# Optimization experiments

Hardware: AMD Instinct MI355X
Metric: run time of the kernel (lower is better)

## Reference

```python
import jax, jax.numpy as jnp
import numpy as np

B, T, EMB, HS = 512, 256, 364, 64

def setup_inputs() -> dict:
    key = jax.random.key(0)
    ks = jax.random.split(key, 7)
    s = EMB ** -0.5  # keep weight scale sane
    return {
        "x": jax.random.normal(ks[0], (B, T, EMB), jnp.float32),
        "Wk": jax.random.normal(ks[1], (EMB, HS), jnp.float32) * s,
        "bk": jax.random.normal(ks[2], (HS,), jnp.float32) * 0.01,
        "Wq": jax.random.normal(ks[3], (EMB, HS), jnp.float32) * s,
        "bq": jax.random.normal(ks[4], (HS,), jnp.float32) * 0.01,
        "Wv": jax.random.normal(ks[5], (EMB, HS), jnp.float32) * s,
        "bv": jax.random.normal(ks[6], (HS,), jnp.float32) * 0.01,
    }

def reference(x, Wk, bk, Wq, bq, Wv, bv):
    # Faithful to the original: wei = k @ q^T (note swapped q/k vs textbook),
    # scaled by head_size**-0.5, causal mask, softmax, (dropout = identity in eval), then @ v.
    k = x @ Wk + bk          # [B, T, HS]
    q = x @ Wq + bq          # [B, T, HS]
    v = x @ Wv + bv          # [B, T, HS]
    scale = k.shape[-1] ** -0.5
    wei = jnp.einsum('btd,bsd->bts', k, q) * scale  # [B, T, T]
    causal = jnp.tril(jnp.ones((T, T), dtype=bool))
    wei = jnp.where(causal, wei, -jnp.inf)
    wei = jax.nn.softmax(wei, axis=-1)
    out = jnp.einsum('bts,bsd->btd', wei, v)        # [B, T, HS]
    return out
```

## Files before the change

### kernel.cpp

```cpp
#include <hip/hip_runtime.h>
#include <math.h>

#define BB   512
#define TT   256
#define EMBD 364
#define HS   64
#define KPAD 384
#define NC   192
#define LDX  136

typedef __attribute__((ext_vector_type(8))) short short8_t;
typedef __attribute__((ext_vector_type(4))) float f32x4;

__device__ __forceinline__ ushort f2bf(float v) {
    union { float f; unsigned u; } c; c.f = v;
    unsigned b = c.u;
    return (ushort)((b + 0x7FFF + ((b >> 16) & 1)) >> 16);
}

__global__ void prep_wt(const float* __restrict__ Wk, const float* __restrict__ Wq,
                        const float* __restrict__ Wv, ushort* __restrict__ WT)
{
    const int c = blockIdx.x;
    const float* Wp = (c < 64) ? Wk : (c < 128 ? Wq : Wv);
    const float s  = (c < 64) ? 0.125f : 1.0f;
    const int col  = c & 63;
    for (int e = threadIdx.x; e < KPAD; e += 64) {
        float v = (e < EMBD) ? Wp[(size_t)e * HS + col] * s : 0.f;
        WT[(size_t)c * KPAD + e] = f2bf(v);
    }
}

#define XSH_OFF 0
#define WSH_OFF (TT * LDX)
#define KB_OFF  0
#define QB_OFF  (TT * 72)
#define VBT_OFF (QB_OFF + TT * 72)
#define PB_OFF  (VBT_OFF + 64 * 264)
#define LDS_USHORT (WSH_OFF + NC * LDX)
#define LDS_BYTES  (LDS_USHORT * 2)

__global__ __launch_bounds__(512, 2) void head_mfma(
    const float* __restrict__ x, const ushort* __restrict__ WT,
    const float* __restrict__ bk_, const float* __restrict__ bq_,
    const float* __restrict__ bv_, float* __restrict__ out)
{
    const int b   = blockIdx.x;
    const int tid = threadIdx.x;
    const int l   = tid & 63;
    const int w   = tid >> 6;
    const int l15 = l & 15;
    const int lg  = l >> 4;

    extern __shared__ ushort sm[];
    ushort* xsh = sm + XSH_OFF;
    ushort* wsh = sm + WSH_OFF;
    ushort* kb  = sm + KB_OFF;
    ushort* qb  = sm + QB_OFF;
    ushort* vbT = sm + VBT_OFF;
    ushort* pbw = sm + PB_OFF + w * (16 * 40);

    const float* xb = x + (size_t)b * TT * EMBD;

    const int nhalf = w & 1;
    const int msub  = w >> 1;

    float bias6[6];
    #pragma unroll
    for (int j = 0; j < 6; ++j) {
        int c = (nhalf * 6 + j) * 16 + l15;
        bias6[j] = (c < 64) ? bk_[c] * 0.125f : (c < 128 ? bq_[c - 64] : bv_[c - 128]);
    }

    f32x4 acc[4][6];
    #pragma unroll
    for (int mi = 0; mi < 4; ++mi)
        #pragma unroll
        for (int j = 0; j < 6; ++j) acc[mi][j] = (f32x4){0.f, 0.f, 0.f, 0.f};

    for (int kc = 0; kc < 3; ++kc) {
        const int K0 = kc * 128;
        __syncthreads();
        #pragma unroll
        for (int it = 0; it < 8; ++it) {
            int r  = it * 32 + (tid >> 4);
            int c8 = (tid & 15) * 8;
            float v[8];
            if (kc < 2) {
                float4 a0 = *(const float4*)&xb[(size_t)r * EMBD + K0 + c8];
                float4 a1 = *(const float4*)&xb[(size_t)r * EMBD + K0 + c8 + 4];
                v[0] = a0.x; v[1] = a0.y; v[2] = a0.z; v[3] = a0.w;
                v[4] = a1.x; v[5] = a1.y; v[6] = a1.z; v[7] = a1.w;
            } else {
                #pragma unroll
                for (int u = 0; u < 8; ++u) {
                    int e = K0 + c8 + u;
                    v[u] = (e < EMBD) ? xb[(size_t)r * EMBD + e] : 0.f;
                }
            }
            union { short8_t s8; ushort us[8]; } pk;
            #pragma unroll
            for (int u = 0; u < 8; ++u) pk.us[u] = f2bf(v[u]);
            *(short8_t*)&xsh[r * LDX + c8] = pk.s8;
        }
        if (tid < 384) {
            int rc = tid >> 1, ch = tid & 1;
            #pragma unroll
            for (int u = 0; u < 8; ++u) {
                short8_t wv = *(const short8_t*)&WT[(size_t)rc * KPAD + K0 + ch * 64 + u * 8];
                *(short8_t*)&wsh[rc * LDX + ch * 64 + u * 8] = wv;
            }
        }
        __syncthreads();
        #pragma unroll
        for (int ks = 0; ks < 4; ++ks) {
            short8_t a[4];
            #pragma unroll
            for (int mi = 0; mi < 4; ++mi)
                a[mi] = *(const short8_t*)&xsh[(mi * 64 + msub * 16 + l15) * LDX + ks * 32 + lg * 8];
            #pragma unroll
            for (int j = 0; j < 6; ++j) {
                short8_t bf = *(const short8_t*)&wsh[((nhalf * 6 + j) * 16 + l15) * LDX + ks * 32 + lg * 8];
                #pragma unroll
                for (int mi = 0; mi < 4; ++mi)
                    acc[mi][j] = __builtin_amdgcn_mfma_f32_16x16x32_bf16(a[mi], bf, acc[mi][j], 0, 0, 0);
            }
        }
    }
    __syncthreads();

    #pragma unroll
    for (int mi = 0; mi < 4; ++mi)
        #pragma unroll
        for (int j = 0; j < 6; ++j) {
            int c = (nhalf * 6 + j) * 16 + l15;
            #pragma unroll
            for (int r = 0; r < 4; ++r) {
                int t = mi * 64 + msub * 16 + lg * 4 + r;
                float val = acc[mi][j][r] + bias6[j];
                if (c < 64)       kb[t * 72 + c]           = f2bf(val);
                else if (c < 128) qb[t * 72 + (c - 64)]    = f2bf(val);
                else              vbT[(c - 128) * 264 + t] = f2bf(val);
            }
        }
    __syncthreads();

    #pragma unroll
    for (int half = 0; half < 2; ++half) {
        const int rt = half ? (15 - w) : w;
        const int t0 = rt * 16;
        float mr[4], lr[4];
        f32x4 o[4];
        #pragma unroll
        for (int r = 0; r < 4; ++r) { mr[r] = -INFINITY; lr[r] = 0.f; }
        #pragma unroll
        for (int nt = 0; nt < 4; ++nt) o[nt] = (f32x4){0.f, 0.f, 0.f, 0.f};

        const int jd = t0 >> 5;
        for (int j = 0; j <= jd; ++j) {
            const int sb = j * 32;
            f32x4 sacc[2];
            sacc[0] = (f32x4){0.f, 0.f, 0.f, 0.f};
            sacc[1] = (f32x4){0.f, 0.f, 0.f, 0.f};
            #pragma unroll
            for (int kk = 0; kk < 2; ++kk) {
                short8_t afr = *(const short8_t*)&kb[(t0 + l15) * 72 + kk * 32 + lg * 8];
                #pragma unroll
                for (int ct = 0; ct < 2; ++ct) {
                    short8_t bfr = *(const short8_t*)&qb[(sb + ct * 16 + l15) * 72 + kk * 32 + lg * 8];
                    sacc[ct] = __builtin_amdgcn_mfma_f32_16x16x32_bf16(afr, bfr, sacc[ct], 0, 0, 0);
                }
            }
            #pragma unroll
            for (int ct = 0; ct < 2; ++ct) {
                int s = sb + ct * 16 + l15;
                #pragma unroll
                for (int r = 0; r < 4; ++r) {
                    int t = t0 + lg * 4 + r;
                    if (s > t) sacc[ct][r] = -INFINITY;
                }
            }
            float p0[4], p1[4], fsc[4];
            #pragma unroll
            for (int r = 0; r < 4; ++r) {
                float mx = fmaxf(sacc[0][r], sacc[1][r]);
                mx = fmaxf(mx, __shfl_xor(mx, 1));
                mx = fmaxf(mx, __shfl_xor(mx, 2));
                mx = fmaxf(mx, __shfl_xor(mx, 4));
                mx = fmaxf(mx, __shfl_xor(mx, 8));
                float nm = fmaxf(mr[r], mx);
                fsc[r] = __expf(mr[r] - nm);
                mr[r] = nm;
                p0[r] = __expf(sacc[0][r] - nm);
                p1[r] = __expf(sacc[1][r] - nm);
                float ps = p0[r] + p1[r];
                ps += __shfl_xor(ps, 1);
                ps += __shfl_xor(ps, 2);
                ps += __shfl_xor(ps, 4);
                ps += __shfl_xor(ps, 8);
                lr[r] = lr[r] * fsc[r] + ps;
            }
            #pragma unroll
            for (int nt = 0; nt < 4; ++nt)
                #pragma unroll
                for (int r = 0; r < 4; ++r) o[nt][r] *= fsc[r];
            #pragma unroll
            for (int r = 0; r < 4; ++r) {
                pbw[(lg * 4 + r) * 40 + l15]      = f2bf(p0[r]);
                pbw[(lg * 4 + r) * 40 + 16 + l15] = f2bf(p1[r]);
            }
            short8_t pa = *(const short8_t*)&pbw[l15 * 40 + lg * 8];
            #pragma unroll
            for (int nt = 0; nt < 4; ++nt) {
                short8_t bfr = *(const short8_t*)&vbT[(nt * 16 + l15) * 264 + sb + lg * 8];
                o[nt] = __builtin_amdgcn_mfma_f32_16x16x32_bf16(pa, bfr, o[nt], 0, 0, 0);
            }
        }
        #pragma unroll
        for (int r = 0; r < 4; ++r) {
            float inv = 1.0f / lr[r];
            int t = t0 + lg * 4 + r;
            float* op = out + ((size_t)b * TT + t) * HS;
            #pragma unroll
            for (int nt = 0; nt < 4; ++nt)
                op[nt * 16 + l15] = o[nt][r] * inv;
        }
    }
}

extern "C" void kernel_launch(void* const* d_in, const int* in_sizes, int n_in,
                              void* d_out, int out_size, void* d_ws, size_t ws_size,
                              hipStream_t stream) {
    const float* x  = (const float*)d_in[0];
    const float* Wk = (const float*)d_in[1];
    const float* bk = (const float*)d_in[2];
    const float* Wq = (const float*)d_in[3];
    const float* bq = (const float*)d_in[4];
    const float* Wv = (const float*)d_in[5];
    const float* bv = (const float*)d_in[6];
    float* out = (float*)d_out;
    ushort* WT = (ushort*)d_ws;

    prep_wt<<<dim3(NC), dim3(64), 0, stream>>>(Wk, Wq, Wv, WT);

    hipFuncSetAttribute((const void*)head_mfma,
                        hipFuncAttributeMaxDynamicSharedMemorySize, LDS_BYTES);
    head_mfma<<<dim3(BB), dim3(512), LDS_BYTES, stream>>>(x, WT, bk, bq, bv, out);
}
```

Before: 114.8 us.

## Split fused head into separate projection GEMM and attention kernels via workspace

When the workspace is large enough, the single fused per-batch kernel becomes two kernels. The first is a projection GEMM over 2048 blocks that reads x straight from global memory into registers and writes bf16 K, Q and transposed V to the workspace. The second is an attention kernel that reads those operands directly from global memory without staging them in LDS, so it uses little shared memory and can run more blocks at once. This trades the large LDS footprint and low occupancy of the fused kernel for an extra global round trip of K/Q/V (about 50 MB) and one more kernel launch.

```diff
diff --git a/kernel.cpp b/kernel.cpp
--- a/kernel.cpp
+++ b/kernel.cpp
@@ -7,7 +7,6 @@
 #define HS   64
 #define KPAD 384
 #define NC   192
-#define LDX  136
 
 typedef __attribute__((ext_vector_type(8))) short short8_t;
 typedef __attribute__((ext_vector_type(4))) float f32x4;
@@ -17,6 +16,13 @@
     unsigned b = c.u;
     return (ushort)((b + 0x7FFF + ((b >> 16) & 1)) >> 16);
 }
+
+#define WT_BYTES  ((size_t)NC * KPAD * 2)
+#define KQ_ELEMS  ((size_t)BB * TT * HS)
+#define K_OFF_B   (WT_BYTES)
+#define Q_OFF_B   (K_OFF_B + KQ_ELEMS * 2)
+#define VT_OFF_B  (Q_OFF_B + KQ_ELEMS * 2)
+#define WS_NEEDED (VT_OFF_B + KQ_ELEMS * 2)
 
 __global__ void prep_wt(const float* __restrict__ Wk, const float* __restrict__ Wq,
                         const float* __restrict__ Wv, ushort* __restrict__ WT)
@@ -31,19 +37,100 @@
     }
 }
 
-#define XSH_OFF 0
-#define WSH_OFF (TT * LDX)
-#define KB_OFF  0
-#define QB_OFF  (TT * 72)
-#define VBT_OFF (QB_OFF + TT * 72)
-#define PB_OFF  (VBT_OFF + 64 * 264)
-#define LDS_USHORT (WSH_OFF + NC * LDX)
-#define LDS_BYTES  (LDS_USHORT * 2)
-
-__global__ __launch_bounds__(512, 2) void head_mfma(
+__global__ __launch_bounds__(256, 4) void proj_gemm(
     const float* __restrict__ x, const ushort* __restrict__ WT,
     const float* __restrict__ bk_, const float* __restrict__ bq_,
-    const float* __restrict__ bv_, float* __restrict__ out)
+    const float* __restrict__ bv_,
+    ushort* __restrict__ Kg, ushort* __restrict__ Qg, ushort* __restrict__ Vt)
+{
+    const int blk = blockIdx.x;
+    const int tid = threadIdx.x;
+    const int l   = tid & 63;
+    const int w   = tid >> 6;
+    const int l15 = l & 15;
+    const int lg  = l >> 4;
+    const int mh  = w >> 1;
+    const int nh  = w & 1;
+
+    const size_t row0 = (size_t)blk * 64 + mh * 32;
+
+    f32x4 acc[2][6];
+    #pragma unroll
+    for (int mi = 0; mi < 2; ++mi)
+        #pragma unroll
+        for (int j = 0; j < 6; ++j) acc[mi][j] = (f32x4){0.f, 0.f, 0.f, 0.f};
+
+    for (int kc = 0; kc < 12; ++kc) {
+        const int k0 = kc * 32;
+        short8_t a[2];
+        if (kc < 11) {
+            #pragma unroll
+            for (int mi = 0; mi < 2; ++mi) {
+                const float* xr = x + (row0 + mi * 16 + l15) * EMBD + k0 + lg * 8;
+                float4 f0 = *(const float4*)xr;
+                float4 f1 = *(const float4*)(xr + 4);
+                union { short8_t s; ushort u[8]; } pk;
+                pk.u[0] = f2bf(f0.x); pk.u[1] = f2bf(f0.y);
+                pk.u[2] = f2bf(f0.z); pk.u[3] = f2bf(f0.w);
+                pk.u[4] = f2bf(f1.x); pk.u[5] = f2bf(f1.y);
+                pk.u[6] = f2bf(f1.z); pk.u[7] = f2bf(f1.w);
+                a[mi] = pk.s;
+            }
+        } else {
+            #pragma unroll
+            for (int mi = 0; mi < 2; ++mi) {
+                const float* xr = x + (row0 + mi * 16 + l15) * EMBD;
+                union { short8_t s; ushort u[8]; } pk;
+                #pragma unroll
+                for (int u2 = 0; u2 < 8; ++u2) {
+                    int k = k0 + lg * 8 + u2;
+                    pk.u[u2] = (k < EMBD) ? f2bf(xr[k]) : (ushort)0;
+                }
+                a[mi] = pk.s;
+            }
+        }
+        #pragma unroll
+        for (int j = 0; j < 6; ++j) {
+            short8_t bf = *(const short8_t*)&WT[(size_t)(nh * 96 + j * 16 + l15) * KPAD + k0 + lg * 8];
+            acc[0][j] = __builtin_amdgcn_mfma_f32_16x16x32_bf16(a[0], bf, acc[0][j], 0, 0, 0);
+            acc[1][j] = __builtin_amdgcn_mfma_f32_16x16x32_bf16(a[1], bf, acc[1][j], 0, 0, 0);
+        }
+    }
+
+    const int b   = blk >> 2;
+    const int tl0 = (blk & 3) * 64 + mh * 32;
+    #pragma unroll
+    for (int j = 0; j < 6; ++j) {
+        const int c = nh * 96 + j * 16 + l15;
+        const float bias = (c < 64) ? bk_[c] * 0.125f
+                         : (c < 128 ? bq_[c - 64] : bv_[c - 128]);
+        #pragma unroll
+        for (int mi = 0; mi < 2; ++mi) {
+            const size_t trow = row0 + mi * 16 + lg * 4;
+            if (c < 64) {
+                #pragma unroll
+                for (int r = 0; r < 4; ++r)
+                    Kg[(trow + r) * HS + c] = f2bf(acc[mi][j][r] + bias);
+            } else if (c < 128) {
+                #pragma unroll
+                for (int r = 0; r < 4; ++r)
+                    Qg[(trow + r) * HS + (c - 64)] = f2bf(acc[mi][j][r] + bias);
+            } else {
+                ushort4 pk;
+                pk.x = f2bf(acc[mi][j][0] + bias);
+                pk.y = f2bf(acc[mi][j][1] + bias);
+                pk.z = f2bf(acc[mi][j][2] + bias);
+                pk.w = f2bf(acc[mi][j][3] + bias);
+                const int tloc = tl0 + mi * 16 + lg * 4;
+                *(ushort4*)&Vt[((size_t)b * HS + (c - 128)) * TT + tloc] = pk;
+            }
+        }
+    }
+}
+
+__global__ __launch_bounds__(512, 4) void attn_fused(
+    const ushort* __restrict__ Kg, const ushort* __restrict__ Qg,
+    const ushort* __restrict__ Vt, float* __restrict__ out)
 {
     const int b   = blockIdx.x;
     const int tid = threadIdx.x;
@@ -52,103 +139,22 @@
     const int l15 = l & 15;
     const int lg  = l >> 4;
 
-    extern __shared__ ushort sm[];
-    ushort* xsh = sm + XSH_OFF;
-    ushort* wsh = sm + WSH_OFF;
-    ushort* kb  = sm + KB_OFF;
-    ushort* qb  = sm + QB_OFF;
-    ushort* vbT = sm + VBT_OFF;
-    ushort* pbw = sm + PB_OFF + w * (16 * 40);
-
-    const float* xb = x + (size_t)b * TT * EMBD;
-
-    const int nhalf = w & 1;
-    const int msub  = w >> 1;
-
-    float bias6[6];
-    #pragma unroll
-    for (int j = 0; j < 6; ++j) {
-        int c = (nhalf * 6 + j) * 16 + l15;
-        bias6[j] = (c < 64) ? bk_[c] * 0.125f : (c < 128 ? bq_[c - 64] : bv_[c - 128]);
-    }
-
-    f32x4 acc[4][6];
-    #pragma unroll
-    for (int mi = 0; mi < 4; ++mi)
-        #pragma unroll
-        for (int j = 0; j < 6; ++j) acc[mi][j] = (f32x4){0.f, 0.f, 0.f, 0.f};
-
-    for (int kc = 0; kc < 3; ++kc) {
-        const int K0 = kc * 128;
-        __syncthreads();
-        #pragma unroll
-        for (int it = 0; it < 8; ++it) {
-            int r  = it * 32 + (tid >> 4);
-            int c8 = (tid & 15) * 8;
-            float v[8];
-            if (kc < 2) {
-                float4 a0 = *(const float4*)&xb[(size_t)r * EMBD + K0 + c8];
-                float4 a1 = *(const float4*)&xb[(size_t)r * EMBD + K0 + c8 + 4];
-                v[0] = a0.x; v[1] = a0.y; v[2] = a0.z; v[3] = a0.w;
-                v[4] = a1.x; v[5] = a1.y; v[6] = a1.z; v[7] = a1.w;
-            } else {
-                #pragma unroll
-                for (int u = 0; u < 8; ++u) {
-                    int e = K0 + c8 + u;
-                    v[u] = (e < EMBD) ? xb[(size_t)r * EMBD + e] : 0.f;
-                }
-            }
-            union { short8_t s8; ushort us[8]; } pk;
-            #pragma unroll
-            for (int u = 0; u < 8; ++u) pk.us[u] = f2bf(v[u]);
-            *(short8_t*)&xsh[r * LDX + c8] = pk.s8;
-        }
-        if (tid < 384) {
-            int rc = tid >> 1, ch = tid & 1;
-            #pragma unroll
-            for (int u = 0; u < 8; ++u) {
-                short8_t wv = *(const short8_t*)&WT[(size_t)rc * KPAD + K0 + ch * 64 + u * 8];
-                *(short8_t*)&wsh[rc * LDX + ch * 64 + u * 8] = wv;
-            }
-        }
-        __syncthreads();
-        #pragma unroll
-        for (int ks = 0; ks < 4; ++ks) {
-            short8_t a[4];
-            #pragma unroll
-            for (int mi = 0; mi < 4; ++mi)
-                a[mi] = *(const short8_t*)&xsh[(mi * 64 + msub * 16 + l15) * LDX + ks * 32 + lg * 8];
-            #pragma unroll
-            for (int j = 0; j < 6; ++j) {
-                short8_t bf = *(const short8_t*)&wsh[((nhalf * 6 + j) * 16 + l15) * LDX + ks * 32 + lg * 8];
-                #pragma unroll
-                for (int mi = 0; mi < 4; ++mi)
-                    acc[mi][j] = __builtin_amdgcn_mfma_f32_16x16x32_bf16(a[mi], bf, acc[mi][j], 0, 0, 0);
-            }
-        }
-    }
-    __syncthreads();
-
-    #pragma unroll
-    for (int mi = 0; mi < 4; ++mi)
-        #pragma unroll
-        for (int j = 0; j < 6; ++j) {
-            int c = (nhalf * 6 + j) * 16 + l15;
-            #pragma unroll
-            for (int r = 0; r < 4; ++r) {
-                int t = mi * 64 + msub * 16 + lg * 4 + r;
-                float val = acc[mi][j][r] + bias6[j];
-                if (c < 64)       kb[t * 72 + c]           = f2bf(val);
-                else if (c < 128) qb[t * 72 + (c - 64)]    = f2bf(val);
-                else              vbT[(c - 128) * 264 + t] = f2bf(val);
-            }
-        }
-    __syncthreads();
+    __shared__ ushort pb[8][16 * 40];
+    ushort* pbw = pb[w];
+
+    const ushort* Kb = Kg + (size_t)b * TT * HS;
+    const ushort* Qb = Qg + (size_t)b * TT * HS;
+    const ushort* Vb = Vt + (size_t)b * HS * TT;
 
     #pragma unroll
     for (int half = 0; half < 2; ++half) {
         const int rt = half ? (15 - w) : w;
         const int t0 = rt * 16;
+
+        short8_t afr[2];
+        afr[0] = *(const short8_t*)&Kb[(t0 + l15) * HS + lg * 8];
+        afr[1] = *(const short8_t*)&Kb[(t0 + l15) * HS + 32 + lg * 8];
+
         float mr[4], lr[4];
         f32x4 o[4];
         #pragma unroll
@@ -164,11 +170,10 @@
             sacc[1] = (f32x4){0.f, 0.f, 0.f, 0.f};
             #pragma unroll
             for (int kk = 0; kk < 2; ++kk) {
-                short8_t afr = *(const short8_t*)&kb[(t0 + l15) * 72 + kk * 32 + lg * 8];
                 #pragma unroll
                 for (int ct = 0; ct < 2; ++ct) {
-                    short8_t bfr = *(const short8_t*)&qb[(sb + ct * 16 + l15) * 72 + kk * 32 + lg * 8];
-                    sacc[ct] = __builtin_amdgcn_mfma_f32_16x16x32_bf16(afr, bfr, sacc[ct], 0, 0, 0);
+                    short8_t bfr = *(const short8_t*)&Qb[(sb + ct * 16 + l15) * HS + kk * 32 + lg * 8];
+                    sacc[ct] = __builtin_amdgcn_mfma_f32_16x16x32_bf16(afr[kk], bfr, sacc[ct], 0, 0, 0);
                 }
             }
             #pragma unroll
@@ -212,6 +217,203 @@
             short8_t pa = *(const short8_t*)&pbw[l15 * 40 + lg * 8];
             #pragma unroll
             for (int nt = 0; nt < 4; ++nt) {
+                short8_t bfr = *(const short8_t*)&Vb[(nt * 16 + l15) * TT + sb + lg * 8];
+                o[nt] = __builtin_amdgcn_mfma_f32_16x16x32_bf16(pa, bfr, o[nt], 0, 0, 0);
+            }
+        }
+        #pragma unroll
+        for (int r = 0; r < 4; ++r) {
+            float inv = 1.0f / lr[r];
+            int t = t0 + lg * 4 + r;
+            float* op = out + ((size_t)b * TT + t) * HS;
+            #pragma unroll
+            for (int nt = 0; nt < 4; ++nt)
+                op[nt * 16 + l15] = o[nt][r] * inv;
+        }
+    }
+}
+
+#define LDX 136
+#define XSH_OFF 0
+#define WSH_OFF (TT * LDX)
+#define KB_OFF  0
+#define QB_OFF  (TT * 72)
+#define VBT_OFF (QB_OFF + TT * 72)
+#define PB_OFF  (VBT_OFF + 64 * 264)
+#define LDS_USHORT (WSH_OFF + NC * LDX)
+#define LDS_BYTES  (LDS_USHORT * 2)
+
+__global__ __launch_bounds__(512, 2) void head_mfma(
+    const float* __restrict__ x, const ushort* __restrict__ WT,
+    const float* __restrict__ bk_, const float* __restrict__ bq_,
+    const float* __restrict__ bv_, float* __restrict__ out)
+{
+    const int b   = blockIdx.x;
+    const int tid = threadIdx.x;
+    const int l   = tid & 63;
+    const int w   = tid >> 6;
+    const int l15 = l & 15;
+    const int lg  = l >> 4;
+
+    extern __shared__ ushort sm[];
+    ushort* xsh = sm + XSH_OFF;
+    ushort* wsh = sm + WSH_OFF;
+    ushort* kb  = sm + KB_OFF;
+    ushort* qb  = sm + QB_OFF;
+    ushort* vbT = sm + VBT_OFF;
+    ushort* pbw = sm + PB_OFF + w * (16 * 40);
+
+    const float* xb = x + (size_t)b * TT * EMBD;
+    const int nhalf = w & 1;
+    const int msub  = w >> 1;
+
+    float bias6[6];
+    #pragma unroll
+    for (int j = 0; j < 6; ++j) {
+        int c = (nhalf * 6 + j) * 16 + l15;
+        bias6[j] = (c < 64) ? bk_[c] * 0.125f : (c < 128 ? bq_[c - 64] : bv_[c - 128]);
+    }
+
+    f32x4 acc[4][6];
+    #pragma unroll
+    for (int mi = 0; mi < 4; ++mi)
+        #pragma unroll
+        for (int j = 0; j < 6; ++j) acc[mi][j] = (f32x4){0.f, 0.f, 0.f, 0.f};
+
+    for (int kc = 0; kc < 3; ++kc) {
+        const int K0 = kc * 128;
+        __syncthreads();
+        #pragma unroll
+        for (int it = 0; it < 8; ++it) {
+            int r  = it * 32 + (tid >> 4);
+            int c8 = (tid & 15) * 8;
+            float v[8];
+            if (kc < 2) {
+                float4 a0 = *(const float4*)&xb[(size_t)r * EMBD + K0 + c8];
+                float4 a1 = *(const float4*)&xb[(size_t)r * EMBD + K0 + c8 + 4];
+                v[0] = a0.x; v[1] = a0.y; v[2] = a0.z; v[3] = a0.w;
+                v[4] = a1.x; v[5] = a1.y; v[6] = a1.z; v[7] = a1.w;
+            } else {
+                #pragma unroll
+                for (int u = 0; u < 8; ++u) {
+                    int e = K0 + c8 + u;
+                    v[u] = (e < EMBD) ? xb[(size_t)r * EMBD + e] : 0.f;
+                }
+            }
+            union { short8_t s8; ushort us[8]; } pk;
+            #pragma unroll
+            for (int u = 0; u < 8; ++u) pk.us[u] = f2bf(v[u]);
+            *(short8_t*)&xsh[r * LDX + c8] = pk.s8;
+        }
+        if (tid < 384) {
+            int rc = tid >> 1, ch = tid & 1;
+            #pragma unroll
+            for (int u = 0; u < 8; ++u) {
+                short8_t wv = *(const short8_t*)&WT[(size_t)rc * KPAD + K0 + ch * 64 + u * 8];
+                *(short8_t*)&wsh[rc * LDX + ch * 64 + u * 8] = wv;
+            }
+        }
+        __syncthreads();
+        #pragma unroll
+        for (int ks = 0; ks < 4; ++ks) {
+            short8_t a[4];
+            #pragma unroll
+            for (int mi = 0; mi < 4; ++mi)
+                a[mi] = *(const short8_t*)&xsh[(mi * 64 + msub * 16 + l15) * LDX + ks * 32 + lg * 8];
+            #pragma unroll
+            for (int j = 0; j < 6; ++j) {
+                short8_t bf = *(const short8_t*)&wsh[((nhalf * 6 + j) * 16 + l15) * LDX + ks * 32 + lg * 8];
+                #pragma unroll
+                for (int mi = 0; mi < 4; ++mi)
+                    acc[mi][j] = __builtin_amdgcn_mfma_f32_16x16x32_bf16(a[mi], bf, acc[mi][j], 0, 0, 0);
+            }
+        }
+    }
+    __syncthreads();
+
+    #pragma unroll
+    for (int mi = 0; mi < 4; ++mi)
+        #pragma unroll
+        for (int j = 0; j < 6; ++j) {
+            int c = (nhalf * 6 + j) * 16 + l15;
+            #pragma unroll
+            for (int r = 0; r < 4; ++r) {
+                int t = mi * 64 + msub * 16 + lg * 4 + r;
+                float val = acc[mi][j][r] + bias6[j];
+                if (c < 64)       kb[t * 72 + c]           = f2bf(val);
+                else if (c < 128) qb[t * 72 + (c - 64)]    = f2bf(val);
+                else              vbT[(c - 128) * 264 + t] = f2bf(val);
+            }
+        }
+    __syncthreads();
+
+    #pragma unroll
+    for (int half = 0; half < 2; ++half) {
+        const int rt = half ? (15 - w) : w;
+        const int t0 = rt * 16;
+        float mr[4], lr[4];
+        f32x4 o[4];
+        #pragma unroll
+        for (int r = 0; r < 4; ++r) { mr[r] = -INFINITY; lr[r] = 0.f; }
+        #pragma unroll
+        for (int nt = 0; nt < 4; ++nt) o[nt] = (f32x4){0.f, 0.f, 0.f, 0.f};
+
+        const int jd = t0 >> 5;
+        for (int j = 0; j <= jd; ++j) {
+            const int sb = j * 32;
+            f32x4 sacc[2];
+            sacc[0] = (f32x4){0.f, 0.f, 0.f, 0.f};
+            sacc[1] = (f32x4){0.f, 0.f, 0.f, 0.f};
+            #pragma unroll
+            for (int kk = 0; kk < 2; ++kk) {
+                short8_t afr = *(const short8_t*)&kb[(t0 + l15) * 72 + kk * 32 + lg * 8];
+                #pragma unroll
+                for (int ct = 0; ct < 2; ++ct) {
+                    short8_t bfr = *(const short8_t*)&qb[(sb + ct * 16 + l15) * 72 + kk * 32 + lg * 8];
+                    sacc[ct] = __builtin_amdgcn_mfma_f32_16x16x32_bf16(afr, bfr, sacc[ct], 0, 0, 0);
+                }
+            }
+            #pragma unroll
+            for (int ct = 0; ct < 2; ++ct) {
+                int s = sb + ct * 16 + l15;
+                #pragma unroll
+                for (int r = 0; r < 4; ++r) {
+                    int t = t0 + lg * 4 + r;
+                    if (s > t) sacc[ct][r] = -INFINITY;
+                }
+            }
+            float p0[4], p1[4], fsc[4];
+            #pragma unroll
+            for (int r = 0; r < 4; ++r) {
+                float mx = fmaxf(sacc[0][r], sacc[1][r]);
+                mx = fmaxf(mx, __shfl_xor(mx, 1));
+                mx = fmaxf(mx, __shfl_xor(mx, 2));
+                mx = fmaxf(mx, __shfl_xor(mx, 4));
+                mx = fmaxf(mx, __shfl_xor(mx, 8));
+                float nm = fmaxf(mr[r], mx);
+                fsc[r] = __expf(mr[r] - nm);
+                mr[r] = nm;
+                p0[r] = __expf(sacc[0][r] - nm);
+                p1[r] = __expf(sacc[1][r] - nm);
+                float ps = p0[r] + p1[r];
+                ps += __shfl_xor(ps, 1);
+                ps += __shfl_xor(ps, 2);
+                ps += __shfl_xor(ps, 4);
+                ps += __shfl_xor(ps, 8);
+                lr[r] = lr[r] * fsc[r] + ps;
+            }
+            #pragma unroll
+            for (int nt = 0; nt < 4; ++nt)
+                #pragma unroll
+                for (int r = 0; r < 4; ++r) o[nt][r] *= fsc[r];
+            #pragma unroll
+            for (int r = 0; r < 4; ++r) {
+                pbw[(lg * 4 + r) * 40 + l15]      = f2bf(p0[r]);
+                pbw[(lg * 4 + r) * 40 + 16 + l15] = f2bf(p1[r]);
+            }
+            short8_t pa = *(const short8_t*)&pbw[l15 * 40 + lg * 8];
+            #pragma unroll
+            for (int nt = 0; nt < 4; ++nt) {
                 short8_t bfr = *(const short8_t*)&vbT[(nt * 16 + l15) * 264 + sb + lg * 8];
                 o[nt] = __builtin_amdgcn_mfma_f32_16x16x32_bf16(pa, bfr, o[nt], 0, 0, 0);
             }
@@ -239,11 +441,19 @@
     const float* Wv = (const float*)d_in[5];
     const float* bv = (const float*)d_in[6];
     float* out = (float*)d_out;
+
     ushort* WT = (ushort*)d_ws;
-
     prep_wt<<<dim3(NC), dim3(64), 0, stream>>>(Wk, Wq, Wv, WT);
 
-    hipFuncSetAttribute((const void*)head_mfma,
-                        hipFuncAttributeMaxDynamicSharedMemorySize, LDS_BYTES);
-    head_mfma<<<dim3(BB), dim3(512), LDS_BYTES, stream>>>(x, WT, bk, bq, bv, out);
-}
+    if (ws_size >= WS_NEEDED) {
+        ushort* Kg = (ushort*)((char*)d_ws + K_OFF_B);
+        ushort* Qg = (ushort*)((char*)d_ws + Q_OFF_B);
+        ushort* Vt = (ushort*)((char*)d_ws + VT_OFF_B);
+        proj_gemm<<<dim3(2048), dim3(256), 0, stream>>>(x, WT, bk, bq, bv, Kg, Qg, Vt);
+        attn_fused<<<dim3(BB), dim3(512), 0, stream>>>(Kg, Qg, Vt, out);
+    } else {
+        hipFuncSetAttribute((const void*)head_mfma,
+                            hipFuncAttributeMaxDynamicSharedMemorySize, LDS_BYTES);
+        head_mfma<<<dim3(BB), dim3(512), LDS_BYTES, stream>>>(x, WT, bk, bq, bv, out);
+    }
+}
```

Result: slower. 169.7 us (+47.8%).

## Split fused head kernel into projection GEMM and attention kernels via workspace

Applied to the files above, without the earlier changes.

The single fused kernel, which projected K/Q/V into LDS and then ran causal attention per batch, is split in two. A separate proj_gemm kernel (2048 blocks of 64 rows) double-buffers x tiles in LDS and writes bf16 K, Q and transposed V to global workspace. The attention kernel then reads K/Q/V from global memory with small LDS use, which should allow higher occupancy. The cost is an extra global round-trip for K/Q/V (about 50MB) plus an extra kernel launch, and the attention kernel's operand loads now come from global memory/cache instead of LDS.

```diff
diff --git a/kernel.cpp b/kernel.cpp
--- a/kernel.cpp
+++ b/kernel.cpp
@@ -7,7 +7,7 @@
 #define HS   64
 #define KPAD 384
 #define NC   192
-#define LDX  136
+#define LP   72
 
 typedef __attribute__((ext_vector_type(8))) short short8_t;
 typedef __attribute__((ext_vector_type(4))) float f32x4;
@@ -17,6 +17,13 @@
     unsigned b = c.u;
     return (ushort)((b + 0x7FFF + ((b >> 16) & 1)) >> 16);
 }
+
+#define WT_BYTES  ((size_t)NC * KPAD * 2)
+#define KQ_ELEMS  ((size_t)BB * TT * HS)
+#define K_OFF_B   (WT_BYTES)
+#define Q_OFF_B   (K_OFF_B + KQ_ELEMS * 2)
+#define VT_OFF_B  (Q_OFF_B + KQ_ELEMS * 2)
+#define WS_NEEDED (VT_OFF_B + KQ_ELEMS * 2)
 
 __global__ void prep_wt(const float* __restrict__ Wk, const float* __restrict__ Wq,
                         const float* __restrict__ Wv, ushort* __restrict__ WT)
@@ -31,19 +38,117 @@
     }
 }
 
-#define XSH_OFF 0
-#define WSH_OFF (TT * LDX)
-#define KB_OFF  0
-#define QB_OFF  (TT * 72)
-#define VBT_OFF (QB_OFF + TT * 72)
-#define PB_OFF  (VBT_OFF + 64 * 264)
-#define LDS_USHORT (WSH_OFF + NC * LDX)
-#define LDS_BYTES  (LDS_USHORT * 2)
-
-__global__ __launch_bounds__(512, 2) void head_mfma(
+__global__ __launch_bounds__(256, 4) void proj_gemm(
     const float* __restrict__ x, const ushort* __restrict__ WT,
     const float* __restrict__ bk_, const float* __restrict__ bq_,
-    const float* __restrict__ bv_, float* __restrict__ out)
+    const float* __restrict__ bv_,
+    ushort* __restrict__ Kg, ushort* __restrict__ Qg, ushort* __restrict__ Vt)
+{
+    const int blk = blockIdx.x;
+    const int tid = threadIdx.x;
+    const int l   = tid & 63;
+    const int w   = tid >> 6;
+    const int l15 = l & 15;
+    const int lg  = l >> 4;
+
+    __shared__ ushort xs[2][64 * LP];
+
+    const float* xb = x + (size_t)blk * 64 * EMBD;
+    const int srow = tid >> 2;
+    const int scol = (tid & 3) * 16;
+
+    float sreg[16];
+
+    auto LOAD = [&](int kc) {
+        const int k0 = kc * 64;
+        if (kc < 5) {
+            #pragma unroll
+            for (int u = 0; u < 4; ++u) {
+                float4 f = *(const float4*)&xb[(size_t)srow * EMBD + k0 + scol + u * 4];
+                sreg[u * 4 + 0] = f.x; sreg[u * 4 + 1] = f.y;
+                sreg[u * 4 + 2] = f.z; sreg[u * 4 + 3] = f.w;
+            }
+        } else {
+            #pragma unroll
+            for (int u = 0; u < 16; ++u) {
+                int k = k0 + scol + u;
+                sreg[u] = (k < EMBD) ? xb[(size_t)srow * EMBD + k] : 0.f;
+            }
+        }
+    };
+    auto WRITE = [&](int buf) {
+        union { short8_t s8; ushort u[8]; } p0, p1;
+        #pragma unroll
+        for (int u = 0; u < 8; ++u) { p0.u[u] = f2bf(sreg[u]); p1.u[u] = f2bf(sreg[8 + u]); }
+        *(short8_t*)&xs[buf][srow * LP + scol]     = p0.s8;
+        *(short8_t*)&xs[buf][srow * LP + scol + 8] = p1.s8;
+    };
+
+    f32x4 acc[4][3];
+    #pragma unroll
+    for (int mi = 0; mi < 4; ++mi)
+        #pragma unroll
+        for (int j = 0; j < 3; ++j) acc[mi][j] = (f32x4){0.f, 0.f, 0.f, 0.f};
+
+    LOAD(0); WRITE(0);
+    __syncthreads();
+
+    for (int kc = 0; kc < 6; ++kc) {
+        if (kc < 5) LOAD(kc + 1);
+        const int buf = kc & 1;
+        #pragma unroll
+        for (int ks = 0; ks < 2; ++ks) {
+            short8_t a[4];
+            #pragma unroll
+            for (int mi = 0; mi < 4; ++mi)
+                a[mi] = *(const short8_t*)&xs[buf][(mi * 16 + l15) * LP + ks * 32 + lg * 8];
+            #pragma unroll
+            for (int j = 0; j < 3; ++j) {
+                const int c = w * 48 + j * 16 + l15;
+                short8_t bf = *(const short8_t*)&WT[(size_t)c * KPAD + kc * 64 + ks * 32 + lg * 8];
+                #pragma unroll
+                for (int mi = 0; mi < 4; ++mi)
+                    acc[mi][j] = __builtin_amdgcn_mfma_f32_16x16x32_bf16(a[mi], bf, acc[mi][j], 0, 0, 0);
+            }
+        }
+        if (kc < 5) WRITE(1 - buf);
+        __syncthreads();
+    }
+
+    const int b   = blk >> 2;
+    const int tl0 = (blk & 3) * 64;
+    #pragma unroll
+    for (int j = 0; j < 3; ++j) {
+        const int c = w * 48 + j * 16 + l15;
+        const float bias = (c < 64) ? bk_[c] * 0.125f
+                         : (c < 128 ? bq_[c - 64] : bv_[c - 128]);
+        #pragma unroll
+        for (int mi = 0; mi < 4; ++mi) {
+            const size_t trow = (size_t)blk * 64 + mi * 16 + lg * 4;
+            if (c < 64) {
+                #pragma unroll
+                for (int r = 0; r < 4; ++r)
+                    Kg[(trow + r) * HS + c] = f2bf(acc[mi][j][r] + bias);
+            } else if (c < 128) {
+                #pragma unroll
+                for (int r = 0; r < 4; ++r)
+                    Qg[(trow + r) * HS + (c - 64)] = f2bf(acc[mi][j][r] + bias);
+            } else {
+                ushort4 pk;
+                pk.x = f2bf(acc[mi][j][0] + bias);
+                pk.y = f2bf(acc[mi][j][1] + bias);
+                pk.z = f2bf(acc[mi][j][2] + bias);
+                pk.w = f2bf(acc[mi][j][3] + bias);
+                const int tloc = tl0 + mi * 16 + lg * 4;
+                *(ushort4*)&Vt[((size_t)b * HS + (c - 128)) * TT + tloc] = pk;
+            }
+        }
+    }
+}
+
+__global__ __launch_bounds__(512, 4) void attn_fused(
+    const ushort* __restrict__ Kg, const ushort* __restrict__ Qg,
+    const ushort* __restrict__ Vt, float* __restrict__ out)
 {
     const int b   = blockIdx.x;
     const int tid = threadIdx.x;
@@ -52,103 +157,22 @@
     const int l15 = l & 15;
     const int lg  = l >> 4;
 
-    extern __shared__ ushort sm[];
-    ushort* xsh = sm + XSH_OFF;
-    ushort* wsh = sm + WSH_OFF;
-    ushort* kb  = sm + KB_OFF;
-    ushort* qb  = sm + QB_OFF;
-    ushort* vbT = sm + VBT_OFF;
-    ushort* pbw = sm + PB_OFF + w * (16 * 40);
-
-    const float* xb = x + (size_t)b * TT * EMBD;
-
-    const int nhalf = w & 1;
-    const int msub  = w >> 1;
-
-    float bias6[6];
-    #pragma unroll
-    for (int j = 0; j < 6; ++j) {
-        int c = (nhalf * 6 + j) * 16 + l15;
-        bias6[j] = (c < 64) ? bk_[c] * 0.125f : (c < 128 ? bq_[c - 64] : bv_[c - 128]);
-    }
-
-    f32x4 acc[4][6];
-    #pragma unroll
-    for (int mi = 0; mi < 4; ++mi)
-        #pragma unroll
-        for (int j = 0; j < 6; ++j) acc[mi][j] = (f32x4){0.f, 0.f, 0.f, 0.f};
-
-    for (int kc = 0; kc < 3; ++kc) {
-        const int K0 = kc * 128;
-        __syncthreads();
-        #pragma unroll
-        for (int it = 0; it < 8; ++it) {
-            int r  = it * 32 + (tid >> 4);
-            int c8 = (tid & 15) * 8;
-            float v[8];
-            if (kc < 2) {
-                float4 a0 = *(const float4*)&xb[(size_t)r * EMBD + K0 + c8];
-                float4 a1 = *(const float4*)&xb[(size_t)r * EMBD + K0 + c8 + 4];
-                v[0] = a0.x; v[1] = a0.y; v[2] = a0.z; v[3] = a0.w;
-                v[4] = a1.x; v[5] = a1.y; v[6] = a1.z; v[7] = a1.w;
-            } else {
-                #pragma unroll
-                for (int u = 0; u < 8; ++u) {
-                    int e = K0 + c8 + u;
-                    v[u] = (e < EMBD) ? xb[(size_t)r * EMBD + e] : 0.f;
-                }
-            }
-            union { short8_t s8; ushort us[8]; } pk;
-            #pragma unroll
-            for (int u = 0; u < 8; ++u) pk.us[u] = f2bf(v[u]);
-            *(short8_t*)&xsh[r * LDX + c8] = pk.s8;
-        }
-        if (tid < 384) {
-            int rc = tid >> 1, ch = tid & 1;
-            #pragma unroll
-            for (int u = 0; u < 8; ++u) {
-                short8_t wv = *(const short8_t*)&WT[(size_t)rc * KPAD + K0 + ch * 64 + u * 8];
-                *(short8_t*)&wsh[rc * LDX + ch * 64 + u * 8] = wv;
-            }
-        }
-        __syncthreads();
-        #pragma unroll
-        for (int ks = 0; ks < 4; ++ks) {
-            short8_t a[4];
-            #pragma unroll
-            for (int mi = 0; mi < 4; ++mi)
-                a[mi] = *(const short8_t*)&xsh[(mi * 64 + msub * 16 + l15) * LDX + ks * 32 + lg * 8];
-            #pragma unroll
-            for (int j = 0; j < 6; ++j) {
-                short8_t bf = *(const short8_t*)&wsh[((nhalf * 6 + j) * 16 + l15) * LDX + ks * 32 + lg * 8];
-                #pragma unroll
-                for (int mi = 0; mi < 4; ++mi)
-                    acc[mi][j] = __builtin_amdgcn_mfma_f32_16x16x32_bf16(a[mi], bf, acc[mi][j], 0, 0, 0);
-            }
-        }
-    }
-    __syncthreads();
-
-    #pragma unroll
-    for (int mi = 0; mi < 4; ++mi)
-        #pragma unroll
-        for (int j = 0; j < 6; ++j) {
-            int c = (nhalf * 6 + j) * 16 + l15;
-            #pragma unroll
-            for (int r = 0; r < 4; ++r) {
-                int t = mi * 64 + msub * 16 + lg * 4 + r;
-                float val = acc[mi][j][r] + bias6[j];
-                if (c < 64)       kb[t * 72 + c]           = f2bf(val);
-                else if (c < 128) qb[t * 72 + (c - 64)]    = f2bf(val);
-                else              vbT[(c - 128) * 264 + t] = f2bf(val);
-            }
-        }
-    __syncthreads();
+    __shared__ ushort pb[8][16 * 40];
+    ushort* pbw = pb[w];
+
+    const ushort* Kb = Kg + (size_t)b * TT * HS;
+    const ushort* Qb = Qg + (size_t)b * TT * HS;
+    const ushort* Vb = Vt + (size_t)b * HS * TT;
 
     #pragma unroll
     for (int half = 0; half < 2; ++half) {
         const int rt = half ? (15 - w) : w;
         const int t0 = rt * 16;
+
+        short8_t afr[2];
+        afr[0] = *(const short8_t*)&Kb[(t0 + l15) * HS + lg * 8];
+        afr[1] = *(const short8_t*)&Kb[(t0 + l15) * HS + 32 + lg * 8];
+
         float mr[4], lr[4];
         f32x4 o[4];
         #pragma unroll
@@ -164,11 +188,10 @@
             sacc[1] = (f32x4){0.f, 0.f, 0.f, 0.f};
             #pragma unroll
             for (int kk = 0; kk < 2; ++kk) {
-                short8_t afr = *(const short8_t*)&kb[(t0 + l15) * 72 + kk * 32 + lg * 8];
                 #pragma unroll
                 for (int ct = 0; ct < 2; ++ct) {
-                    short8_t bfr = *(const short8_t*)&qb[(sb + ct * 16 + l15) * 72 + kk * 32 + lg * 8];
-                    sacc[ct] = __builtin_amdgcn_mfma_f32_16x16x32_bf16(afr, bfr, sacc[ct], 0, 0, 0);
+                    short8_t bfr = *(const short8_t*)&Qb[(sb + ct * 16 + l15) * HS + kk * 32 + lg * 8];
+                    sacc[ct] = __builtin_amdgcn_mfma_f32_16x16x32_bf16(afr[kk], bfr, sacc[ct], 0, 0, 0);
                 }
             }
             #pragma unroll
@@ -212,7 +235,7 @@
             short8_t pa = *(const short8_t*)&pbw[l15 * 40 + lg * 8];
             #pragma unroll
             for (int nt = 0; nt < 4; ++nt) {
-                short8_t bfr = *(const short8_t*)&vbT[(nt * 16 + l15) * 264 + sb + lg * 8];
+                short8_t bfr = *(const short8_t*)&Vb[(nt * 16 + l15) * TT + sb + lg * 8];
                 o[nt] = __builtin_amdgcn_mfma_f32_16x16x32_bf16(pa, bfr, o[nt], 0, 0, 0);
             }
         }
@@ -239,11 +262,13 @@
     const float* Wv = (const float*)d_in[5];
     const float* bv = (const float*)d_in[6];
     float* out = (float*)d_out;
+
     ushort* WT = (ushort*)d_ws;
+    ushort* Kg = (ushort*)((char*)d_ws + K_OFF_B);
+    ushort* Qg = (ushort*)((char*)d_ws + Q_OFF_B);
+    ushort* Vt = (ushort*)((char*)d_ws + VT_OFF_B);
 
     prep_wt<<<dim3(NC), dim3(64), 0, stream>>>(Wk, Wq, Wv, WT);
-
-    hipFuncSetAttribute((const void*)head_mfma,
-                        hipFuncAttributeMaxDynamicSharedMemorySize, LDS_BYTES);
-    head_mfma<<<dim3(BB), dim3(512), LDS_BYTES, stream>>>(x, WT, bk, bq, bv, out);
-}
+    proj_gemm<<<dim3(2048), dim3(256), 0, stream>>>(x, WT, bk, bq, bv, Kg, Qg, Vt);
+    attn_fused<<<dim3(BB), dim3(512), 0, stream>>>(Kg, Qg, Vt, out);
+}
```

Measured after the change: 128.0 us. +11.6%, slower.
